# Optimization experiments

Measured on AMD Instinct MI355X. Metric: run time of the kernel, lower is better.

The kernel has to match this reference:

```python
import jax, jax.numpy as jnp
import numpy as np

COMMITMENT_WEIGHT = 1.0


def setup_inputs() -> dict:
    key = jax.random.key(0)
    k1, k2 = jax.random.split(key)
    clap_embeddings = jax.random.normal(k1, (16, 2048, 512), dtype=jnp.float32)
    # Learned codebooks for the 8 residual quantizer stages: [Q, C, D]
    codebooks = jax.random.normal(k2, (8, 1024, 512), dtype=jnp.float32)
    return {"clap_embeddings": clap_embeddings, "codebooks": codebooks}


def reference(clap_embeddings, codebooks):
    """Residual VQ: cascade of nearest-codebook lookups on the residual.
    Returns (quantized [B,T,D], indices [B,T,Q], commit_loss scalar)."""
    B, T, D = clap_embeddings.shape
    flat = clap_embeddings.reshape(-1, D)  # [N, D], N = B*T

    def step(carry, cb):
        residual, quant_acc = carry          # [N,D], [N,D]; cb: [C,D]
        cb_sq = jnp.sum(cb * cb, axis=-1)    # [C]
        # squared-dist argmin: ||r||^2 term is constant per row, drop it
        dists = cb_sq[None, :] - 2.0 * (residual @ cb.T)  # [N, C]
        idx = jnp.argmin(dists, axis=-1)     # [N]
        qv = cb[idx]                         # [N, D] gather
        # commitment loss: mse(detach(quantize), residual_input)
        loss = jnp.mean(jnp.square(jax.lax.stop_gradient(qv) - residual))
        # straight-through estimator
        qv_st = residual + jax.lax.stop_gradient(qv - residual)
        new_residual = residual - jax.lax.stop_gradient(qv)
        return (new_residual, quant_acc + qv_st), (idx, loss)

    init = (flat, jnp.zeros_like(flat))
    (_, quant_flat), (idx_q, losses) = jax.lax.scan(step, init, codebooks)

    quantized = quant_flat.reshape(B, T, D)
    indices = jnp.transpose(idx_q, (1, 0)).reshape(B, T, -1)  # [B, T, Q]
    commit_loss = jnp.sum(losses) * COMMITMENT_WEIGHT
    return quantized, indices, commit_loss
```

## Files before the change

### kernel.cpp

```cpp
#include <hip/hip_runtime.h>
#include <hip/hip_bf16.h>

#define NQ 8
#define NC 1024
#define ND 512
#define NROWTOT 32768
#define QOFF 16777216ULL

typedef short short8 __attribute__((ext_vector_type(8)));
typedef float f32x16 __attribute__((ext_vector_type(16)));

__device__ __forceinline__ unsigned f2bf_u(float f) {
  unsigned u = __float_as_uint(f);
  return (u + 0x7FFFu + ((u >> 16) & 1u)) >> 16;
}
__device__ __forceinline__ void merge_in(float &d1, int &i1, float &d2, int &i2,
                                         float nd, int ni) {
  bool b1 = (nd < d1) || (nd == d1 && ni < i1);
  bool b2 = (nd < d2) || (nd == d2 && ni < i2);
  if (b1) { d2 = d1; i2 = i1; d1 = nd; i1 = ni; }
  else if (b2) { d2 = nd; i2 = ni; }
}

__global__ __launch_bounds__(256) void cbsq_kernel(const float* __restrict__ cbg,
                                                   float* __restrict__ ws) {
  const int tid = threadIdx.x, wv = tid >> 6, lane = tid & 63;
  const int cbase = blockIdx.x * 32 + wv * 8;
  for (int j = 0; j < 8; ++j) {
    const int c = cbase + j;
    const float4* p = reinterpret_cast<const float4*>(cbg + (size_t)c * ND + lane * 8);
    float4 a = p[0], b = p[1];
    float s = a.x*a.x + a.y*a.y + a.z*a.z + a.w*a.w
            + b.x*b.x + b.y*b.y + b.z*b.z + b.w*b.w;
    #pragma unroll
    for (int m = 1; m < 64; m <<= 1) s += __shfl_xor(s, m, 64);
    if (lane == 0) ws[c] = s;
  }
}

__global__ __launch_bounds__(256) void fmt_kernel(const float* __restrict__ cbg,
                                                  unsigned short* __restrict__ Bh,
                                                  unsigned short* __restrict__ Bl) {
  int t = blockIdx.x * 256 + threadIdx.x;
  int i16 = t & 1023, ks = (t >> 10) & 31, cp = (t >> 15) & 1, q = (t >> 16) & 7;
  int grp = i16 >> 9, col = i16 & 511, c = cp * 512 + col;
  const float* src = cbg + ((size_t)q * NC + c) * ND + ks * 16 + grp * 8;
  float4 a = reinterpret_cast<const float4*>(src)[0];
  float4 b = reinterpret_cast<const float4*>(src)[1];
  float v[8] = {a.x, a.y, a.z, a.w, b.x, b.y, b.z, b.w};
  unsigned short hv[8], lv[8];
  #pragma unroll
  for (int j = 0; j < 8; ++j) {
    unsigned hb = f2bf_u(v[j]);
    float hf = __uint_as_float(hb << 16);
    unsigned lb = f2bf_u(v[j] - hf);
    hv[j] = (unsigned short)hb; lv[j] = (unsigned short)lb;
  }
  int phys = i16 ^ ((i16 >> 3) & 7);
  size_t dst = (size_t)(t >> 10) * 8192 + (size_t)phys * 8;
  uint4 wh, wl;
  wh.x = hv[0] | ((unsigned)hv[1] << 16); wh.y = hv[2] | ((unsigned)hv[3] << 16);
  wh.z = hv[4] | ((unsigned)hv[5] << 16); wh.w = hv[6] | ((unsigned)hv[7] << 16);
  wl.x = lv[0] | ((unsigned)lv[1] << 16); wl.y = lv[2] | ((unsigned)lv[3] << 16);
  wl.z = lv[4] | ((unsigned)lv[5] << 16); wl.w = lv[6] | ((unsigned)lv[7] << 16);
  *reinterpret_cast<uint4*>(Bh + dst) = wh;
  *reinterpret_cast<uint4*>(Bl + dst) = wl;
}

#define ROWS64 64
#define RSTRIDE 260
#define TAU2 0.02f

__global__ __launch_bounds__(1024, 4) void rvq_mfma(
    const float* __restrict__ emb, const float* __restrict__ cbg,
    const float* __restrict__ cbsq_g, float* __restrict__ lossws,
    const unsigned short* __restrict__ Bh, const unsigned short* __restrict__ Bl,
    float* __restrict__ outf) {
  __shared__ unsigned resH[ROWS64 * RSTRIDE];
  __shared__ unsigned resL[ROWS64 * RSTRIDE];
  __shared__ float mrgd[2][8][ROWS64][2];
  __shared__ int   mrgi[2][8][ROWS64][2];
  __shared__ int   idx_all[NQ][ROWS64];
  __shared__ int   fi_sh[ROWS64];
  __shared__ int   tlist[ROWS64][3];
  __shared__ int   tcount;
  __shared__ float wred[16];

  const int tid = threadIdx.x;
  const int w = tid >> 6, l = tid & 63;
  const int n0 = blockIdx.x * ROWS64;
  const int rowbase = (w >> 3) * 32;
  const int colq = (w & 7) * 64;
  const int arow = rowbase + (l & 31);
  const int phase = blockIdx.x & 31;
  const int cpswap = (blockIdx.x >> 5) & 1;

  union U8 { uint4 q4; short8 s; };

  const int row = tid & 63, kb0i = (tid >> 6) * 16;

  {
    const float4* src = reinterpret_cast<const float4*>(emb + (size_t)(n0 + row) * ND + kb0i * 2);
    float4 v8[8];
    #pragma unroll
    for (int i = 0; i < 8; ++i) v8[i] = src[i];
    #pragma unroll
    for (int j = 0; j < 4; ++j) {
      float vv[8];
      vv[0]=v8[2*j].x; vv[1]=v8[2*j].y; vv[2]=v8[2*j].z; vv[3]=v8[2*j].w;
      vv[4]=v8[2*j+1].x; vv[5]=v8[2*j+1].y; vv[6]=v8[2*j+1].z; vv[7]=v8[2*j+1].w;
      unsigned hh[8], ll[8];
      #pragma unroll
      for (int e = 0; e < 8; ++e) {
        hh[e] = f2bf_u(vv[e]);
        ll[e] = f2bf_u(vv[e] - __uint_as_float(hh[e] << 16));
      }
      uint4 H, L;
      H.x = hh[0] | (hh[1] << 16); H.y = hh[2] | (hh[3] << 16);
      H.z = hh[4] | (hh[5] << 16); H.w = hh[6] | (hh[7] << 16);
      L.x = ll[0] | (ll[1] << 16); L.y = ll[2] | (ll[3] << 16);
      L.z = ll[4] | (ll[5] << 16); L.w = ll[6] | (ll[7] << 16);
      const int off = row * RSTRIDE + kb0i + 4 * j;
      *reinterpret_cast<uint4*>(&resH[off]) = H;
      *reinterpret_cast<uint4*>(&resL[off]) = L;
    }
  }

  int baddr[2];
  #pragma unroll
  for (int t = 0; t < 2; ++t) {
    int i16 = ((l >> 5) << 9) + colq + t * 32 + (l & 31);
    baddr[t] = (i16 ^ ((i16 >> 3) & 7)) * 8;
  }
  const int kbh = (l >> 5) * 4;
  const int abase = arow * RSTRIDE;
  __syncthreads();

  for (int q = 0; q < NQ; ++q) {
    if (tid == 0) tcount = 0;

    #pragma unroll 1
    for (int cpi = 0; cpi < 2; ++cpi) {
      const int cp = cpi ^ cpswap;
      f32x16 acc[2];
      #pragma unroll
      for (int t = 0; t < 2; ++t)
        #pragma unroll
        for (int e = 0; e < 16; ++e) acc[t][e] = 0.f;

      const unsigned short* bhc = Bh + (size_t)((q * 2 + cp) * 32) * 8192;
      const unsigned short* blc = Bl + (size_t)((q * 2 + cp) * 32) * 8192;
      uint4 fA[4], fB[4];
      uint4 aAh, aAl, aBh, aBl;

      float sqv[2];
      #pragma unroll
      for (int t = 0; t < 2; ++t)
        sqv[t] = cbsq_g[q * NC + cp * 512 + colq + t * 32 + (l & 31)];

#define KS(i) (((i) + phase) & 31)

#define LOADB(buf, kk) { \
      const unsigned short* _h = bhc + (size_t)(kk) * 8192; \
      const unsigned short* _l = blc + (size_t)(kk) * 8192; \
      buf[0] = *reinterpret_cast<const uint4*>(_h + baddr[0]); \
      buf[1] = *reinterpret_cast<const uint4*>(_h + baddr[1]); \
      buf[2] = *reinterpret_cast<const uint4*>(_l + baddr[0]); \
      buf[3] = *reinterpret_cast<const uint4*>(_l + baddr[1]); }

#define READA(ah_, al_, kk) { \
      const int _a = abase + (kk) * 8 + kbh; \
      ah_ = *reinterpret_cast<const uint4*>(&resH[_a]); \
      al_ = *reinterpret_cast<const uint4*>(&resL[_a]); }

#define MFMAS(ah_, al_, buf) { \
      U8 A1, A2; A1.q4 = ah_; A2.q4 = al_; \
      _Pragma("unroll") \
      for (int t = 0; t < 2; ++t) { \
        U8 bh_, bl_; bh_.q4 = buf[t]; bl_.q4 = buf[2 + t]; \
        acc[t] = __builtin_amdgcn_mfma_f32_32x32x16_bf16(A1.s, bh_.s, acc[t], 0, 0, 0); \
        acc[t] = __builtin_amdgcn_mfma_f32_32x32x16_bf16(A2.s, bh_.s, acc[t], 0, 0, 0); \
        acc[t] = __builtin_amdgcn_mfma_f32_32x32x16_bf16(A1.s, bl_.s, acc[t], 0, 0, 0); \
      } }

      LOADB(fA, KS(0)); LOADB(fB, KS(1)); READA(aAh, aAl, KS(0));
      #pragma unroll 1
      for (int ks = 0; ks < 32; ks += 2) {
        READA(aBh, aBl, KS(ks + 1));
        MFMAS(aAh, aAl, fA);
        LOADB(fA, KS(ks + 2));
        READA(aAh, aAl, KS(ks + 2));
        MFMAS(aBh, aBl, fB);
        LOADB(fB, KS(ks + 3));
      }
#undef LOADB
#undef READA
#undef MFMAS
#undef KS

      #pragma unroll
      for (int rg2 = 0; rg2 < 16; ++rg2) {
        float d1 = INFINITY, d2 = INFINITY; int i1 = 0x7fffffff, i2 = 0x7fffffff;
        #pragma unroll
        for (int t = 0; t < 2; ++t) {
          int col = cp * 512 + colq + t * 32 + (l & 31);
          float dd = sqv[t] - 2.0f * acc[t][rg2];
          merge_in(d1, i1, d2, i2, dd, col);
        }
        #pragma unroll
        for (int m = 1; m < 32; m <<= 1) {
          float od1 = __shfl_xor(d1, m, 64), od2 = __shfl_xor(d2, m, 64);
          int oi1 = __shfl_xor(i1, m, 64), oi2 = __shfl_xor(i2, m, 64);
          merge_in(d1, i1, d2, i2, od1, oi1);
          merge_in(d1, i1, d2, i2, od2, oi2);
        }
        if ((l & 31) == 0) {
          int h = l >> 5;
          int rr = rowbase + (rg2 & 3) + 8 * (rg2 >> 2) + 4 * h;
          mrgd[cp][w & 7][rr][0] = d1; mrgd[cp][w & 7][rr][1] = d2;
          mrgi[cp][w & 7][rr][0] = i1; mrgi[cp][w & 7][rr][1] = i2;
        }
      }
    }
    __syncthreads();

    if (tid < ROWS64) {
      float d1 = INFINITY, d2 = INFINITY; int i1 = 0x7fffffff, i2 = 0x7fffffff;
      #pragma unroll
      for (int c2 = 0; c2 < 2; ++c2)
        #pragma unroll
        for (int s2 = 0; s2 < 8; ++s2) {
          merge_in(d1, i1, d2, i2, mrgd[c2][s2][tid][0], mrgi[c2][s2][tid][0]);
          merge_in(d1, i1, d2, i2, mrgd[c2][s2][tid][1], mrgi[c2][s2][tid][1]);
        }
      int fi = i1 < 0 ? 0 : (i1 > NC - 1 ? NC - 1 : i1);
      int ib = i2 < 0 ? 0 : (i2 > NC - 1 ? NC - 1 : i2);
      fi_sh[tid] = fi;
      if (d2 - d1 < TAU2 && ib != fi) {
        int p = atomicAdd(&tcount, 1);
        tlist[p][0] = tid; tlist[p][1] = fi; tlist[p][2] = ib;
      }
    }
    __syncthreads();

    {
      int nt_ = tcount;
      for (int it = w; it < nt_; it += 16) {
        int rr = tlist[it][0], ia = tlist[it][1], ib = tlist[it][2];
        float rv[8];
        const float4* ep = reinterpret_cast<const float4*>(emb + (size_t)(n0 + rr) * ND + l * 8);
        float4 e0 = ep[0], e1 = ep[1];
        rv[0]=e0.x; rv[1]=e0.y; rv[2]=e0.z; rv[3]=e0.w;
        rv[4]=e1.x; rv[5]=e1.y; rv[6]=e1.z; rv[7]=e1.w;
        for (int t2 = 0; t2 < q; ++t2) {
          const float4* cr = reinterpret_cast<const float4*>(
              cbg + ((size_t)t2 * NC + idx_all[t2][rr]) * ND + l * 8);
          float4 c0 = cr[0], c1 = cr[1];
          rv[0]-=c0.x; rv[1]-=c0.y; rv[2]-=c0.z; rv[3]-=c0.w;
          rv[4]-=c1.x; rv[5]-=c1.y; rv[6]-=c1.z; rv[7]-=c1.w;
        }
        double da = 0.0, db = 0.0;
        {
          const float4* cr = reinterpret_cast<const float4*>(
              cbg + ((size_t)q * NC + ia) * ND + l * 8);
          float4 c0 = cr[0], c1 = cr[1];
          float cv[8] = {c0.x,c0.y,c0.z,c0.w,c1.x,c1.y,c1.z,c1.w};
          #pragma unroll
          for (int j = 0; j < 8; ++j) { double e = (double)cv[j] - (double)rv[j]; da += e * e; }
        }
        {
          const float4* cr = reinterpret_cast<const float4*>(
              cbg + ((size_t)q * NC + ib) * ND + l * 8);
          float4 c0 = cr[0], c1 = cr[1];
          float cv[8] = {c0.x,c0.y,c0.z,c0.w,c1.x,c1.y,c1.z,c1.w};
          #pragma unroll
          for (int j = 0; j < 8; ++j) { double e = (double)cv[j] - (double)rv[j]; db += e * e; }
        }
        #pragma unroll
        for (int m = 1; m < 64; m <<= 1) { da += __shfl_xor(da, m, 64); db += __shfl_xor(db, m, 64); }
        if (l == 0 && (db < da || (db == da && ib < ia))) fi_sh[rr] = ib;
      }
    }
    __syncthreads();

    if (tid < ROWS64) {
      idx_all[q][tid] = fi_sh[tid];
      outf[QOFF + (size_t)(n0 + tid) * NQ + q] = (float)fi_sh[tid];
    }

    {
      const float* crow = cbg + ((size_t)q * NC + fi_sh[row]) * ND;
      const float4* cp4 = reinterpret_cast<const float4*>(crow + kb0i * 2);
      const float4* ep4 = reinterpret_cast<const float4*>(emb + (size_t)(n0 + row) * ND + kb0i * 2);
      float4* op4 = reinterpret_cast<float4*>(outf + (size_t)(n0 + row) * ND + kb0i * 2);
      float4 cv8[8];
      #pragma unroll
      for (int u2 = 0; u2 < 8; ++u2) cv8[u2] = cp4[u2];
      float ls = 0.f;
      #pragma unroll
      for (int j = 0; j < 4; ++j) {
        const int off = row * RSTRIDE + kb0i + 4 * j;
        uint4 H = *reinterpret_cast<const uint4*>(&resH[off]);
        uint4 L = *reinterpret_cast<const uint4*>(&resL[off]);
        unsigned hu[4] = {H.x, H.y, H.z, H.w};
        unsigned lu[4] = {L.x, L.y, L.z, L.w};
        float cf[8];
        cf[0]=cv8[2*j].x; cf[1]=cv8[2*j].y; cf[2]=cv8[2*j].z; cf[3]=cv8[2*j].w;
        cf[4]=cv8[2*j+1].x; cf[5]=cv8[2*j+1].y; cf[6]=cv8[2*j+1].z; cf[7]=cv8[2*j+1].w;
        float x[8];
        #pragma unroll
        for (int e = 0; e < 4; ++e) {
          float rlo = __uint_as_float(hu[e] << 16) + __uint_as_float(lu[e] << 16);
          float rhi = __uint_as_float(hu[e] & 0xFFFF0000u) + __uint_as_float(lu[e] & 0xFFFF0000u);
          x[2*e]   = rlo - cf[2*e];
          x[2*e+1] = rhi - cf[2*e+1];
        }
        unsigned nh[4], nl[4];
        #pragma unroll
        for (int e = 0; e < 4; ++e) {
          unsigned h0 = f2bf_u(x[2*e]);
          unsigned l0 = f2bf_u(x[2*e] - __uint_as_float(h0 << 16));
          unsigned h1 = f2bf_u(x[2*e+1]);
          unsigned l1 = f2bf_u(x[2*e+1] - __uint_as_float(h1 << 16));
          nh[e] = h0 | (h1 << 16);
          nl[e] = l0 | (l1 << 16);
          ls += x[2*e] * x[2*e] + x[2*e+1] * x[2*e+1];
        }
        uint4 NH, NL;
        NH.x = nh[0]; NH.y = nh[1]; NH.z = nh[2]; NH.w = nh[3];
        NL.x = nl[0]; NL.y = nl[1]; NL.z = nl[2]; NL.w = nl[3];
        *reinterpret_cast<uint4*>(&resH[off]) = NH;
        *reinterpret_cast<uint4*>(&resL[off]) = NL;
        if (q == NQ - 1) {
          float4 e0 = ep4[2*j], e1 = ep4[2*j+1];
          float4 q0, q1;
          q0.x = e0.x - x[0]; q0.y = e0.y - x[1]; q0.z = e0.z - x[2]; q0.w = e0.w - x[3];
          q1.x = e1.x - x[4]; q1.y = e1.y - x[5]; q1.z = e1.z - x[6]; q1.w = e1.w - x[7];
          op4[2*j] = q0; op4[2*j+1] = q1;
        }
      }
      #pragma unroll
      for (int m = 1; m < 64; m <<= 1) ls += __shfl_xor(ls, m, 64);
      if (l == 0) wred[w] = ls;
    }
    __syncthreads();
    if (tid == 0) {
      float s = 0.f;
      #pragma unroll
      for (int i = 0; i < 16; ++i) s += wred[i];
      lossws[blockIdx.x * NQ + q] = s;
    }
    __syncthreads();
  }
}

#define ROWS 32
#define BK 32
#define CP 512
#define TAU 0.05f

__global__ __launch_bounds__(256, 1) void rvq_fb(
    const float* __restrict__ emb, const float* __restrict__ cbg,
    const float* __restrict__ cbsq, float* __restrict__ lossws,
    float* __restrict__ outf) {
  __shared__ float resT[ND][ROWS];
  __shared__ float cc[BK][CP];
  __shared__ int   idx_sh[ROWS];
  __shared__ float wred[4];

  const int tid = threadIdx.x;
  const int wv = tid >> 6, lane = tid & 63;
  const int rg = wv, cg = lane;
  const int n0 = blockIdx.x * ROWS;

  float qacc[64];
  #pragma unroll
  for (int s = 0; s < 64; ++s) qacc[s] = 0.f;

  {
    const int r = tid & 31, db = tid >> 5;
    const float4* src = reinterpret_cast<const float4*>(emb + (size_t)(n0 + r) * ND + db * 64);
    #pragma unroll
    for (int s = 0; s < 16; ++s) {
      float4 v = src[s];
      int d = db * 64 + s * 4;
      resT[d+0][r] = v.x; resT[d+1][r] = v.y; resT[d+2][r] = v.z; resT[d+3][r] = v.w;
    }
  }
  __syncthreads();

  const int c0l = cg * 8;
  const int swm = (c0l >> 6) << 2;
  const int off0 = c0l ^ swm;
  const int off1 = (c0l + 4) ^ swm;

  for (int q = 0; q < NQ; ++q) {
    const float* cbq = cbg + (size_t)q * NC * ND;
    float bd1[8], bd2[8]; int bi1[8], bi2[8];
    #pragma unroll
    for (int j = 0; j < 8; ++j) { bd1[j]=INFINITY; bd2[j]=INFINITY; bi1[j]=0x7fffffff; bi2[j]=0x7fffffff; }

    for (int cp = 0; cp < 2; ++cp) {
      float acc[8][8];
      #pragma unroll
      for (int a = 0; a < 8; ++a)
        #pragma unroll
        for (int b = 0; b < 8; ++b) acc[a][b] = 0.f;

      for (int kc = 0; kc < ND / BK; ++kc) {
        __syncthreads();
        {
          const int half = tid & 1;
          const int k0 = half * 16;
          #pragma unroll
          for (int it = 0; it < 4; ++it) {
            const int c = (tid >> 1) + it * 128;
            const int pc = c ^ ((c >> 6) << 2);
            const float4* src = reinterpret_cast<const float4*>(
                cbq + (size_t)(cp * CP + c) * ND + kc * BK + half * 16);
            float4 v0 = src[0], v1 = src[1], v2 = src[2], v3 = src[3];
            cc[k0+ 0][pc]=v0.x; cc[k0+ 1][pc]=v0.y; cc[k0+ 2][pc]=v0.z; cc[k0+ 3][pc]=v0.w;
            cc[k0+ 4][pc]=v1.x; cc[k0+ 5][pc]=v1.y; cc[k0+ 6][pc]=v1.z; cc[k0+ 7][pc]=v1.w;
            cc[k0+ 8][pc]=v2.x; cc[k0+ 9][pc]=v2.y; cc[k0+10][pc]=v2.z; cc[k0+11][pc]=v2.w;
            cc[k0+12][pc]=v3.x; cc[k0+13][pc]=v3.y; cc[k0+14][pc]=v3.z; cc[k0+15][pc]=v3.w;
          }
        }
        __syncthreads();

        float tmp[8][8];
        #pragma unroll
        for (int a = 0; a < 8; ++a)
          #pragma unroll
          for (int b = 0; b < 8; ++b) tmp[a][b] = 0.f;

        #pragma unroll
        for (int kk = 0; kk < BK; ++kk) {
          const float4* rp = reinterpret_cast<const float4*>(&resT[kc * BK + kk][rg * 8]);
          float4 r0 = rp[0], r1 = rp[1];
          const float* ccrow = &cc[kk][0];
          float4 c0 = *reinterpret_cast<const float4*>(ccrow + off0);
          float4 c1 = *reinterpret_cast<const float4*>(ccrow + off1);
          float rv[8] = {r0.x, r0.y, r0.z, r0.w, r1.x, r1.y, r1.z, r1.w};
          float cv[8] = {c0.x, c0.y, c0.z, c0.w, c1.x, c1.y, c1.z, c1.w};
          #pragma unroll
          for (int a = 0; a < 8; ++a)
            #pragma unroll
            for (int b = 0; b < 8; ++b)
              tmp[a][b] = fmaf(rv[a], cv[b], tmp[a][b]);
        }
        #pragma unroll
        for (int a = 0; a < 8; ++a)
          #pragma unroll
          for (int b = 0; b < 8; ++b) acc[a][b] += tmp[a][b];
      }

      const float4* qp = reinterpret_cast<const float4*>(cbsq + q * NC + cp * CP + cg * 8);
      float4 s0 = qp[0], s1 = qp[1];
      float sqv[8] = {s0.x, s0.y, s0.z, s0.w, s1.x, s1.y, s1.z, s1.w};
      #pragma unroll
      for (int r = 0; r < 8; ++r) {
        float d1 = INFINITY, d2 = INFINITY; int i1 = 0x7fffffff, i2 = 0x7fffffff;
        #pragma unroll
        for (int j = 0; j < 8; ++j) {
          float dd = sqv[j] - 2.0f * acc[r][j];
          merge_in(d1, i1, d2, i2, dd, cp * CP + cg * 8 + j);
        }
        #pragma unroll
        for (int m = 1; m < 64; m <<= 1) {
          float od1 = __shfl_xor(d1, m, 64), od2 = __shfl_xor(d2, m, 64);
          int oi1 = __shfl_xor(i1, m, 64), oi2 = __shfl_xor(i2, m, 64);
          merge_in(d1, i1, d2, i2, od1, oi1);
          merge_in(d1, i1, d2, i2, od2, oi2);
        }
        merge_in(bd1[r], bi1[r], bd2[r], bi2[r], d1, i1);
        merge_in(bd1[r], bi1[r], bd2[r], bi2[r], d2, i2);
      }
    }

    #pragma unroll 1
    for (int r = 0; r < 8; ++r) {
      int fi = bi1[r];
      if (bd2[r] - bd1[r] < TAU) {
        const int row = rg * 8 + r;
        const int ia = bi1[r], ib = bi2[r];
        double da = 0.0, db2 = 0.0;
        #pragma unroll 1
        for (int t = 0; t < 2; ++t) {
          const int cidx = t ? ib : ia;
          const float* cr = cbq + (size_t)cidx * ND;
          double dot = 0.0, ss = 0.0;
          #pragma unroll
          for (int u = 0; u < 8; ++u) {
            int k = lane * 8 + u;
            double cvv = (double)cr[k];
            double rvv = (double)resT[k][row];
            dot += cvv * rvv; ss += cvv * cvv;
          }
          #pragma unroll
          for (int m = 1; m < 64; m <<= 1) { dot += __shfl_xor(dot, m, 64); ss += __shfl_xor(ss, m, 64); }
          double dd = ss - 2.0 * dot;
          if (t) db2 = dd; else da = dd;
        }
        if (db2 < da || (db2 == da && ib < ia)) fi = ib;
      }
      fi = fi < 0 ? 0 : (fi > NC - 1 ? NC - 1 : fi);
      if (lane == 0) {
        idx_sh[rg * 8 + r] = fi;
        outf[QOFF + (size_t)(n0 + rg * 8 + r) * NQ + q] = (float)fi;
      }
    }
    __syncthreads();

    {
      const int r = tid & 31, db = tid >> 5;
      const float* crow = cbq + (size_t)idx_sh[r] * ND;
      float ls = 0.f;
      #pragma unroll
      for (int s = 0; s < 64; ++s) {
        int d = db * 64 + s;
        float cv = crow[d];
        float nv = resT[d][r] - cv;
        resT[d][r] = nv;
        qacc[s] += cv;
        ls += nv * nv;
      }
      #pragma unroll
      for (int m = 1; m < 64; m <<= 1) ls += __shfl_xor(ls, m, 64);
      if (lane == 0) wred[wv] = ls;
    }
    __syncthreads();
    if (tid == 0) lossws[blockIdx.x * NQ + q] = wred[0] + wred[1] + wred[2] + wred[3];
    __syncthreads();
  }

  {
    const int r = tid & 31, db = tid >> 5;
    #pragma unroll
    for (int g = 0; g < 16; ++g) {
      float4 w2;
      w2.x = qacc[g*4+0]; w2.y = qacc[g*4+1]; w2.z = qacc[g*4+2]; w2.w = qacc[g*4+3];
      *reinterpret_cast<float4*>(outf + (size_t)(n0 + r) * ND + db * 64 + g * 4) = w2;
    }
  }
}

__global__ __launch_bounds__(256) void loss_kernel(const float* __restrict__ lossws,
                                                   int n, float* __restrict__ outf) {
  __shared__ float red[256];
  const int tid = threadIdx.x;
  float s = 0.f;
  for (int i = tid; i < n; i += 256) s += lossws[i];
  red[tid] = s;
  __syncthreads();
  for (int w = 128; w > 0; w >>= 1) {
    if (tid < w) red[tid] += red[tid + w];
    __syncthreads();
  }
  if (tid == 0) outf[QOFF + (size_t)NROWTOT * NQ] = red[0] / 16777216.0f;
}

extern "C" void kernel_launch(void* const* d_in, const int* in_sizes, int n_in,
                              void* d_out, int out_size, void* d_ws, size_t ws_size,
                              hipStream_t stream) {
  (void)in_sizes; (void)n_in; (void)out_size;
  const float* emb = (const float*)d_in[0];
  const float* cbg = (const float*)d_in[1];
  float* wsf = (float*)d_ws;
  float* outf = (float*)d_out;

  cbsq_kernel<<<256, 256, 0, stream>>>(cbg, wsf);

  if (ws_size >= (size_t)18 * 1024 * 1024) {
    unsigned short* Bh = (unsigned short*)((char*)d_ws + 65536);
    unsigned short* Bl = Bh + 4194304;
    fmt_kernel<<<2048, 256, 0, stream>>>(cbg, Bh, Bl);
    rvq_mfma<<<512, 1024, 0, stream>>>(emb, cbg, wsf, wsf + 8192, Bh, Bl, outf);
    loss_kernel<<<1, 256, 0, stream>>>(wsf + 8192, 4096, outf);
  } else {
    rvq_fb<<<1024, 256, 0, stream>>>(emb, cbg, wsf, wsf + 8192, outf);
    loss_kernel<<<1, 256, 0, stream>>>(wsf + 8192, 8192, outf);
  }
}
```

Measured before the change: 3.976 ms.

## Stage codebook chunks into LDS via async global_load_lds with 32-row blocks

```diff
diff --git a/kernel.cpp b/kernel.cpp
--- a/kernel.cpp
+++ b/kernel.cpp
@@ -67,40 +67,46 @@
   *reinterpret_cast<uint4*>(Bl + dst) = wl;
 }
 
-#define ROWS64 64
+#define ROWS32 32
 #define RSTRIDE 260
 #define TAU2 0.02f
 
-__global__ __launch_bounds__(1024, 4) void rvq_mfma(
+__device__ __forceinline__ int chunk_of(int n, int cpswap, int phase) {
+  int qn = n >> 6, cpin = (n >> 5) & 1, ksn = n & 31;
+  return ((qn * 2 + (cpin ^ cpswap)) * 32) + ((ksn + phase) & 31);
+}
+
+__global__ __launch_bounds__(512, 2) void rvq_mfma(
     const float* __restrict__ emb, const float* __restrict__ cbg,
     const float* __restrict__ cbsq_g, float* __restrict__ lossws,
     const unsigned short* __restrict__ Bh, const unsigned short* __restrict__ Bl,
     float* __restrict__ outf) {
-  __shared__ unsigned resH[ROWS64 * RSTRIDE];
-  __shared__ unsigned resL[ROWS64 * RSTRIDE];
-  __shared__ float mrgd[2][8][ROWS64][2];
-  __shared__ int   mrgi[2][8][ROWS64][2];
-  __shared__ int   idx_all[NQ][ROWS64];
-  __shared__ int   fi_sh[ROWS64];
-  __shared__ int   tlist[ROWS64][3];
+  __shared__ unsigned resH[ROWS32 * RSTRIDE];
+  __shared__ unsigned resL[ROWS32 * RSTRIDE];
+  __shared__ uint4 Bbuf[2][2048];
+  __shared__ float mrgd[2][8][ROWS32][2];
+  __shared__ int   mrgi[2][8][ROWS32][2];
+  __shared__ int   idx_all[NQ][ROWS32];
+  __shared__ int   fi_sh[ROWS32];
+  __shared__ int   tlist[ROWS32][3];
   __shared__ int   tcount;
-  __shared__ float wred[16];
+  __shared__ float wred[8];
 
   const int tid = threadIdx.x;
   const int w = tid >> 6, l = tid & 63;
-  const int n0 = blockIdx.x * ROWS64;
-  const int rowbase = (w >> 3) * 32;
-  const int colq = (w & 7) * 64;
-  const int arow = rowbase + (l & 31);
+  const int n0 = blockIdx.x * ROWS32;
+  const int colq = w * 64;
+  const int arow = l & 31;
   const int phase = blockIdx.x & 31;
   const int cpswap = (blockIdx.x >> 5) & 1;
 
   union U8 { uint4 q4; short8 s; };
 
-  const int row = tid & 63, kb0i = (tid >> 6) * 16;
+  const int row = tid & 31, seg = tid >> 5;
+  const int kb0i = seg * 16;
 
   {
-    const float4* src = reinterpret_cast<const float4*>(emb + (size_t)(n0 + row) * ND + kb0i * 2);
+    const float4* src = reinterpret_cast<const float4*>(emb + (size_t)(n0 + row) * ND + seg * 32);
     float4 v8[8];
     #pragma unroll
     for (int i = 0; i < 8; ++i) v8[i] = src[i];
@@ -126,14 +132,30 @@
     }
   }
 
-  int baddr[2];
+  int bb[2];
   #pragma unroll
   for (int t = 0; t < 2; ++t) {
     int i16 = ((l >> 5) << 9) + colq + t * 32 + (l & 31);
-    baddr[t] = (i16 ^ ((i16 >> 3) & 7)) * 8;
+    bb[t] = (i16 ^ ((i16 >> 3) & 7)) * 16;
   }
   const int kbh = (l >> 5) * 4;
   const int abase = arow * RSTRIDE;
+
+#define STAGE(c, b) { \
+    const char* _hs = (const char*)(Bh + (size_t)(c) * 8192) + (w << 11) + (l << 4); \
+    const char* _ls = (const char*)(Bl + (size_t)(c) * 8192) + (w << 11) + (l << 4); \
+    char* _ld = (char*)&Bbuf[(b)][0] + (w << 11); \
+    __builtin_amdgcn_global_load_lds((const __attribute__((address_space(1))) void*)_hs, \
+        (__attribute__((address_space(3))) void*)_ld, 16, 0, 0); \
+    __builtin_amdgcn_global_load_lds((const __attribute__((address_space(1))) void*)(_hs + 1024), \
+        (__attribute__((address_space(3))) void*)(_ld + 1024), 16, 0, 0); \
+    __builtin_amdgcn_global_load_lds((const __attribute__((address_space(1))) void*)_ls, \
+        (__attribute__((address_space(3))) void*)(_ld + 16384), 16, 0, 0); \
+    __builtin_amdgcn_global_load_lds((const __attribute__((address_space(1))) void*)(_ls + 1024), \
+        (__attribute__((address_space(3))) void*)(_ld + 17408), 16, 0, 0); \
+  }
+
+  STAGE(chunk_of(0, cpswap, phase), 0);
   __syncthreads();
 
   for (int q = 0; q < NQ; ++q) {
@@ -148,55 +170,37 @@
         #pragma unroll
         for (int e = 0; e < 16; ++e) acc[t][e] = 0.f;
 
-      const unsigned short* bhc = Bh + (size_t)((q * 2 + cp) * 32) * 8192;
-      const unsigned short* blc = Bl + (size_t)((q * 2 + cp) * 32) * 8192;
-      uint4 fA[4], fB[4];
-      uint4 aAh, aAl, aBh, aBl;
-
       float sqv[2];
       #pragma unroll
       for (int t = 0; t < 2; ++t)
         sqv[t] = cbsq_g[q * NC + cp * 512 + colq + t * 32 + (l & 31)];
 
-#define KS(i) (((i) + phase) & 31)
-
-#define LOADB(buf, kk) { \
-      const unsigned short* _h = bhc + (size_t)(kk) * 8192; \
-      const unsigned short* _l = blc + (size_t)(kk) * 8192; \
-      buf[0] = *reinterpret_cast<const uint4*>(_h + baddr[0]); \
-      buf[1] = *reinterpret_cast<const uint4*>(_h + baddr[1]); \
-      buf[2] = *reinterpret_cast<const uint4*>(_l + baddr[0]); \
-      buf[3] = *reinterpret_cast<const uint4*>(_l + baddr[1]); }
-
-#define READA(ah_, al_, kk) { \
-      const int _a = abase + (kk) * 8 + kbh; \
-      ah_ = *reinterpret_cast<const uint4*>(&resH[_a]); \
-      al_ = *reinterpret_cast<const uint4*>(&resL[_a]); }
-
-#define MFMAS(ah_, al_, buf) { \
-      U8 A1, A2; A1.q4 = ah_; A2.q4 = al_; \
-      _Pragma("unroll") \
-      for (int t = 0; t < 2; ++t) { \
-        U8 bh_, bl_; bh_.q4 = buf[t]; bl_.q4 = buf[2 + t]; \
-        acc[t] = __builtin_amdgcn_mfma_f32_32x32x16_bf16(A1.s, bh_.s, acc[t], 0, 0, 0); \
-        acc[t] = __builtin_amdgcn_mfma_f32_32x32x16_bf16(A2.s, bh_.s, acc[t], 0, 0, 0); \
-        acc[t] = __builtin_amdgcn_mfma_f32_32x32x16_bf16(A1.s, bl_.s, acc[t], 0, 0, 0); \
-      } }
-
-      LOADB(fA, KS(0)); LOADB(fB, KS(1)); READA(aAh, aAl, KS(0));
       #pragma unroll 1
-      for (int ks = 0; ks < 32; ks += 2) {
-        READA(aBh, aBl, KS(ks + 1));
-        MFMAS(aAh, aAl, fA);
-        LOADB(fA, KS(ks + 2));
-        READA(aAh, aAl, KS(ks + 2));
-        MFMAS(aBh, aBl, fB);
-        LOADB(fB, KS(ks + 3));
-      }
-#undef LOADB
-#undef READA
-#undef MFMAS
-#undef KS
+      for (int ksi = 0; ksi < 32; ++ksi) {
+        const int n = q * 64 + cpi * 32 + ksi;
+        if (n + 1 < 512) STAGE(chunk_of(n + 1, cpswap, phase), (n + 1) & 1);
+
+        const int kk = (ksi + phase) & 31;
+        const int a = abase + kk * 8 + kbh;
+        U8 Ah, Al;
+        Ah.q4 = *reinterpret_cast<const uint4*>(&resH[a]);
+        Al.q4 = *reinterpret_cast<const uint4*>(&resL[a]);
+
+        const char* bp = (const char*)&Bbuf[n & 1][0];
+        U8 B0h, B1h, B0l, B1l;
+        B0h.q4 = *reinterpret_cast<const uint4*>(bp + bb[0]);
+        B1h.q4 = *reinterpret_cast<const uint4*>(bp + bb[1]);
+        B0l.q4 = *reinterpret_cast<const uint4*>(bp + 16384 + bb[0]);
+        B1l.q4 = *reinterpret_cast<const uint4*>(bp + 16384 + bb[1]);
+
+        acc[0] = __builtin_amdgcn_mfma_f32_32x32x16_bf16(Ah.s, B0h.s, acc[0], 0, 0, 0);
+        acc[0] = __builtin_amdgcn_mfma_f32_32x32x16_bf16(Al.s, B0h.s, acc[0], 0, 0, 0);
+        acc[0] = __builtin_amdgcn_mfma_f32_32x32x16_bf16(Ah.s, B0l.s, acc[0], 0, 0, 0);
+        acc[1] = __builtin_amdgcn_mfma_f32_32x32x16_bf16(Ah.s, B1h.s, acc[1], 0, 0, 0);
+        acc[1] = __builtin_amdgcn_mfma_f32_32x32x16_bf16(Al.s, B1h.s, acc[1], 0, 0, 0);
+        acc[1] = __builtin_amdgcn_mfma_f32_32x32x16_bf16(Ah.s, B1l.s, acc[1], 0, 0, 0);
+        __syncthreads();
+      }
 
       #pragma unroll
       for (int rg2 = 0; rg2 < 16; ++rg2) {
@@ -216,15 +220,15 @@
         }
         if ((l & 31) == 0) {
           int h = l >> 5;
-          int rr = rowbase + (rg2 & 3) + 8 * (rg2 >> 2) + 4 * h;
-          mrgd[cp][w & 7][rr][0] = d1; mrgd[cp][w & 7][rr][1] = d2;
-          mrgi[cp][w & 7][rr][0] = i1; mrgi[cp][w & 7][rr][1] = i2;
-        }
-      }
-    }
-    __syncthreads();
-
-    if (tid < ROWS64) {
+          int rr = (rg2 & 3) + 8 * (rg2 >> 2) + 4 * h;
+          mrgd[cp][w][rr][0] = d1; mrgd[cp][w][rr][1] = d2;
+          mrgi[cp][w][rr][0] = i1; mrgi[cp][w][rr][1] = i2;
+        }
+      }
+    }
+    __syncthreads();
+
+    if (tid < ROWS32) {
       float d1 = INFINITY, d2 = INFINITY; int i1 = 0x7fffffff, i2 = 0x7fffffff;
       #pragma unroll
       for (int c2 = 0; c2 < 2; ++c2)
@@ -245,7 +249,7 @@
 
     {
       int nt_ = tcount;
-      for (int it = w; it < nt_; it += 16) {
+      for (int it = w; it < nt_; it += 8) {
         int rr = tlist[it][0], ia = tlist[it][1], ib = tlist[it][2];
         float rv[8];
         const float4* ep = reinterpret_cast<const float4*>(emb + (size_t)(n0 + rr) * ND + l * 8);
@@ -283,16 +287,16 @@
     }
     __syncthreads();
 
-    if (tid < ROWS64) {
+    if (tid < ROWS32) {
       idx_all[q][tid] = fi_sh[tid];
       outf[QOFF + (size_t)(n0 + tid) * NQ + q] = (float)fi_sh[tid];
     }
 
     {
       const float* crow = cbg + ((size_t)q * NC + fi_sh[row]) * ND;
-      const float4* cp4 = reinterpret_cast<const float4*>(crow + kb0i * 2);
-      const float4* ep4 = reinterpret_cast<const float4*>(emb + (size_t)(n0 + row) * ND + kb0i * 2);
-      float4* op4 = reinterpret_cast<float4*>(outf + (size_t)(n0 + row) * ND + kb0i * 2);
+      const float4* cp4 = reinterpret_cast<const float4*>(crow + seg * 32);
+      const float4* ep4 = reinterpret_cast<const float4*>(emb + (size_t)(n0 + row) * ND + seg * 32);
+      float4* op4 = reinterpret_cast<float4*>(outf + (size_t)(n0 + row) * ND + seg * 32);
       float4 cv8[8];
       #pragma unroll
       for (int u2 = 0; u2 < 8; ++u2) cv8[u2] = cp4[u2];
@@ -347,11 +351,12 @@
     if (tid == 0) {
       float s = 0.f;
       #pragma unroll
-      for (int i = 0; i < 16; ++i) s += wred[i];
+      for (int i = 0; i < 8; ++i) s += wred[i];
       lossws[blockIdx.x * NQ + q] = s;
     }
     __syncthreads();
   }
+#undef STAGE
 }
 
 #define ROWS 32
@@ -574,8 +579,8 @@
     unsigned short* Bh = (unsigned short*)((char*)d_ws + 65536);
     unsigned short* Bl = Bh + 4194304;
     fmt_kernel<<<2048, 256, 0, stream>>>(cbg, Bh, Bl);
-    rvq_mfma<<<512, 1024, 0, stream>>>(emb, cbg, wsf, wsf + 8192, Bh, Bl, outf);
-    loss_kernel<<<1, 256, 0, stream>>>(wsf + 8192, 4096, outf);
+    rvq_mfma<<<1024, 512, 0, stream>>>(emb, cbg, wsf, wsf + 8192, Bh, Bl, outf);
+    loss_kernel<<<1, 256, 0, stream>>>(wsf + 8192, 8192, outf);
   } else {
     rvq_fb<<<1024, 256, 0, stream>>>(emb, cbg, wsf, wsf + 8192, outf);
     loss_kernel<<<1, 256, 0, stream>>>(wsf + 8192, 8192, outf);
```

Result: slower. 5.639 ms (+41.8%).
